# Kernel tuning notes

Measured on AMD Instinct MI355X. Metric: run time of the kernel, lower is better.

The kernel has to match this reference:

```python
import jax, jax.numpy as jnp
import numpy as np

B, P, L, H = 64, 1024, 16, 256
NUM_SIZE = 18
TOPK = min(64, P)


def _ramp(epoch, a, b):
    if epoch <= a:
        return 0.0
    if epoch >= b:
        return 1.0
    return float(epoch - a) / float(b - a)


def _normalize(x):
    return x / jnp.maximum(jnp.linalg.norm(x, axis=-1, keepdims=True), 1e-12)


def setup_inputs() -> dict:
    key = jax.random.key(0)
    ks = jax.random.split(key, 16)
    return {
        'pred_center': jax.random.normal(ks[0], (B, P, 3), dtype=jnp.float32),
        'pred_size': jax.random.uniform(ks[1], (B, P, 3), minval=0.2, maxval=1.0, dtype=jnp.float32),
        'bbox_feature': jax.random.normal(ks[2], (B, P, H), dtype=jnp.float32),
        'objectness_scores': jax.random.normal(ks[3], (B, P, 2), dtype=jnp.float32),
        'lang_emb': jax.random.normal(ks[4], (B * L, H), dtype=jnp.float32),
        'lang_num': jax.random.randint(ks[5], (B,), 1, L + 1),
        'ref_center': jax.random.normal(ks[6], (B, L, 3), dtype=jnp.float32),
        'ref_size_class': jax.random.randint(ks[7], (B, L), 0, NUM_SIZE),
        'ref_size_residual': jax.random.uniform(ks[8], (B, L, 3), minval=0.0, maxval=0.2, dtype=jnp.float32),
        'mean_size_arr': jax.random.uniform(ks[9], (NUM_SIZE, 3), minval=0.3, maxval=1.5, dtype=jnp.float32),
        'W_text': jax.random.normal(ks[10], (H, H), dtype=jnp.float32) / np.sqrt(H),
        'W_pc': jax.random.normal(ks[11], (H, H), dtype=jnp.float32) / np.sqrt(H),
        'W_pc_iou': jax.random.normal(ks[12], (H, H), dtype=jnp.float32) / np.sqrt(H),
        'log_inv_tau': jnp.array([np.log(1.0 / 0.07)], dtype=jnp.float32),
        'epoch': 40,
    }


def _forward(pred_center, pred_size, bbox_feature, objectness_scores, lang_emb,
             lang_num, ref_center, ref_size_class, ref_size_residual,
             mean_size_arr, W_text, W_pc, W_pc_iou, log_inv_tau, epoch):
    b, l = ref_center.shape[:2]
    # curriculum (python scalars, epoch is a static int)
    p = _ramp(epoch, 0, 80)
    thr = 0.05 + 0.3 * p
    gamma = 1.0 + 2.0 * p
    min_tau = 0.08 - 0.04 * p

    # top-k proposals by objectness prob
    obj_prob = jax.nn.softmax(objectness_scores, axis=2)[..., 1]  # (B,P)
    _, topk_inds = jax.lax.top_k(obj_prob, TOPK)                  # (B,K)
    feat = jnp.take_along_axis(bbox_feature, topk_inds[..., None], axis=1)  # (B,K,H)
    ctr = jnp.take_along_axis(pred_center, topk_inds[..., None], axis=1)    # (B,K,3)
    sz = jnp.take_along_axis(pred_size, topk_inds[..., None], axis=1)       # (B,K,3)

    # axis-aligned 3D IoU between gt boxes (B,L) and pred boxes (B,K) -- detached
    gt_size = mean_size_arr[ref_size_class] + ref_size_residual + 0.01  # (B,L,3)
    gmin, gmax = ref_center - gt_size / 2, ref_center + gt_size / 2
    pmin, pmax = ctr - sz / 2, ctr + sz / 2
    lo = jnp.maximum(gmin[:, :, None], pmin[:, None])   # (B,L,K,3)
    hi = jnp.minimum(gmax[:, :, None], pmax[:, None])
    inter = jnp.prod(jnp.clip(hi - lo, 0.0, None), axis=-1)  # (B,L,K)
    vol_g = jnp.prod(gt_size, axis=-1)[:, :, None]
    vol_p = jnp.prod(sz, axis=-1)[:, None]
    iou = jax.lax.stop_gradient(inter / (vol_g + vol_p - inter + 1e-7))  # (B,L,K)

    # soft target over proposals (detached)
    w = jnp.clip(iou, 0.0, None) ** gamma * (iou >= thr).astype(iou.dtype)
    onehot = jax.nn.one_hot(jnp.argmax(iou, axis=-1), TOPK, dtype=iou.dtype)
    w = jnp.where(w.sum(-1, keepdims=True) < 1e-6, onehot, w)
    target = w / (w.sum(-1, keepdims=True) + 1e-6)  # (B,L,K)

    # temperature
    inv_tau = jnp.minimum(jnp.exp(log_inv_tau)[0], 100.0)
    inv_tau = jnp.minimum(inv_tau, 1.0 / max(min_tau, 1e-6))

    # language-box contrastive
    text = _normalize(lang_emb.reshape(b, l, -1) @ W_text.T)  # (B,L,H)
    boxf = _normalize(feat @ W_pc.T)                          # (B,K,H)
    sim = jnp.einsum('blh,bkh->blk', text, boxf)              # (B,L,K)
    logp = jax.nn.log_softmax(sim * inv_tau, axis=-1)
    t2 = target / (target.sum(-1, keepdims=True) + 1e-6)      # soft_ce renorm
    ce = -(t2 * logp).sum(-1)                                 # (B,L)

    neg = iou < 0.05
    s_neg = jnp.max(jnp.where(neg, sim, -jnp.inf), axis=-1)
    s_pos = (sim * target).sum(-1)
    rank = jnp.where(neg.any(-1), jax.nn.relu(0.2 - s_pos + s_neg), 0.0)
    lang_con = ce + 0.5 * rank                                # (B,L)

    mask = (jnp.arange(l)[None, :] < lang_num[:, None]).astype(sim.dtype)
    lang_loss = (lang_con * mask).sum() / b

    # iou-aware box-box contrastive
    tm = w[..., :, None] * w[..., None, :]                    # (B,L,K,K) detached
    tm = tm / (tm.sum(-1, keepdims=True) + 1e-6)
    tm = tm / (tm.sum(-1, keepdims=True) + 1e-6)              # soft_ce renorm
    boxf_iou = _normalize(feat @ W_pc_iou.T)                  # (B,K,H)
    sim_iou = jnp.einsum('bkh,bmh->bkm', boxf_iou, boxf_iou)  # (B,K,K)
    logp_iou = jax.nn.log_softmax(sim_iou * inv_tau, axis=-1)
    iou_ce = -(tm * logp_iou[:, None]).sum(-1).mean(-1)       # (B,L)
    iou_loss = (iou_ce * mask).sum() / b

    return jnp.stack([lang_loss, iou_loss])


def reference(pred_center, pred_size, bbox_feature, objectness_scores, lang_emb,
              lang_num, ref_center, ref_size_class, ref_size_residual,
              mean_size_arr, W_text, W_pc, W_pc_iou, log_inv_tau, epoch):
    return _forward(pred_center, pred_size, bbox_feature, objectness_scores,
                    lang_emb, lang_num, ref_center, ref_size_class,
                    ref_size_residual, mean_size_arr, W_text, W_pc, W_pc_iou,
                    log_inv_tau, epoch)
```

## Files before the change

### kernel.cpp

```cpp
#include <hip/hip_runtime.h>
#include <math.h>

#define B 64
#define P 1024
#define L 16
#define H 256
#define K 64

__device__ __forceinline__ float wsum(float v){
  #pragma unroll
  for (int o = 32; o >= 1; o >>= 1) v += __shfl_xor(v, o, 64);
  return v;
}
__device__ __forceinline__ float wmaxr(float v){
  #pragma unroll
  for (int o = 32; o >= 1; o >>= 1) v = fmaxf(v, __shfl_xor(v, o, 64));
  return v;
}
__device__ __forceinline__ void wargmax(float &v, int &i){
  #pragma unroll
  for (int o = 32; o >= 1; o >>= 1){
    float v2 = __shfl_xor(v, o, 64);
    int   i2 = __shfl_xor(i, o, 64);
    if (v2 > v || (v2 == v && i2 < i)){ v = v2; i = i2; }
  }
}
__device__ __forceinline__ unsigned fkey(float f){
  unsigned b = __float_as_uint(f);
  return (b & 0x80000000u) ? ~b : (b | 0x80000000u);
}
__device__ __forceinline__ float dot4(float4 a, float4 b){
  return a.x*b.x + a.y*b.y + a.z*b.z + a.w*b.w;
}
__device__ __forceinline__ int gsw(int r){ return (r ^ (r >> 3)) & 7; }

__global__ __launch_bounds__(256) void k_topk_iou(
    const float* __restrict__ pred_center, const float* __restrict__ pred_size,
    const float* __restrict__ obj, const float* __restrict__ ref_center,
    const int* __restrict__ ref_cls, const float* __restrict__ ref_res,
    const float* __restrict__ mean_sz, const int* __restrict__ epoch_p,
    const int* __restrict__ lang_num,
    int* __restrict__ inds, float* __restrict__ iou_ws, float* __restrict__ w_ws,
    float* __restrict__ c_ws, float* __restrict__ t_ws, float* __restrict__ t2_ws,
    float* __restrict__ t2s_ws)
{
  __shared__ int hist[256];
  __shared__ int s_digit, s_cum;
  __shared__ int waveTot[4];
  __shared__ int sel[K];
  __shared__ float ctrS[K][3], szS[K][3];
  int b = blockIdx.x, tid = threadIdx.x, lane = tid & 63, wave = tid >> 6;

  const float4* o4 = (const float4*)(obj + (size_t)b*P*2);
  float4 va = o4[tid*2], vb = o4[tid*2+1];
  unsigned kj[4] = { fkey(va.y - va.x), fkey(va.w - va.z),
                     fkey(vb.y - vb.x), fkey(vb.w - vb.z) };

  unsigned prefix = 0; int rem = K;
  for (int pass = 0; pass < 4; ++pass){
    int shift = 24 - pass*8;
    hist[tid] = 0;
    __syncthreads();
    #pragma unroll
    for (int j = 0; j < 4; ++j){
      unsigned kk = kj[j];
      bool cand = (pass == 0) || ((kk >> (shift + 8)) == prefix);
      if (cand) atomicAdd(&hist[(kk >> shift) & 0xff], 1);
    }
    __syncthreads();
    int d = 255 - tid;
    int h = hist[d];
    int s = h;
    #pragma unroll
    for (int o = 1; o < 64; o <<= 1){ int t = __shfl_up(s, o, 64); if (lane >= o) s += t; }
    if (lane == 63) waveTot[wave] = s;
    __syncthreads();
    #pragma unroll
    for (int q = 0; q < 3; ++q) if (q < wave) s += waveTot[q];
    if (s >= rem && s - h < rem){ s_digit = d; s_cum = s - h; }
    __syncthreads();
    prefix = (prefix << 8) | (unsigned)s_digit;
    rem -= s_cum;
    __syncthreads();
  }
  unsigned T = prefix;
  int remFinal = rem;

  int eqc = 0;
  #pragma unroll
  for (int j = 0; j < 4; ++j) eqc += (kj[j] == T) ? 1 : 0;
  int v = eqc;
  #pragma unroll
  for (int o = 1; o < 64; o <<= 1){ int t = __shfl_up(v, o, 64); if (lane >= o) v += t; }
  if (lane == 63) waveTot[wave] = v;
  __syncthreads();
  int off = 0;
  for (int q = 0; q < wave; ++q) off += waveTot[q];
  int e = off + v - eqc;
  __syncthreads();

  int selc = 0; bool ch[4];
  #pragma unroll
  for (int j = 0; j < 4; ++j){
    bool g = kj[j] > T;
    bool q = (kj[j] == T) && (e < remFinal);
    if (kj[j] == T) e++;
    ch[j] = g || q; selc += ch[j] ? 1 : 0;
  }
  v = selc;
  #pragma unroll
  for (int o = 1; o < 64; o <<= 1){ int t = __shfl_up(v, o, 64); if (lane >= o) v += t; }
  if (lane == 63) waveTot[wave] = v;
  __syncthreads();
  off = 0;
  for (int q = 0; q < wave; ++q) off += waveTot[q];
  int slot = off + v - selc;
  #pragma unroll
  for (int j = 0; j < 4; ++j) if (ch[j]) sel[slot++] = tid*4 + j;
  __syncthreads();

  if (tid < K){
    int idx = sel[tid];
    inds[b*K + tid] = idx;
    #pragma unroll
    for (int dd = 0; dd < 3; ++dd){
      ctrS[tid][dd] = pred_center[((size_t)b*P + idx)*3 + dd];
      szS [tid][dd] = pred_size [((size_t)b*P + idx)*3 + dd];
    }
  }
  __syncthreads();

  int ep = epoch_p[0];
  float pr = ep <= 0 ? 0.f : (ep >= 80 ? 1.f : ep / 80.f);
  float thr = 0.05f + 0.3f * pr;
  float gamma = 1.f + 2.f * pr;
  int ln = lang_num[b];

  for (int l = wave; l < L; l += 4){
    int cls = ref_cls[b*L + l];
    float gs[3], gc[3]; float volg = 1.f;
    #pragma unroll
    for (int dd = 0; dd < 3; ++dd){
      gs[dd] = mean_sz[cls*3+dd] + ref_res[((size_t)b*L+l)*3+dd] + 0.01f;
      gc[dd] = ref_center[((size_t)b*L+l)*3+dd];
      volg *= gs[dd];
    }
    int k = lane;
    float inter = 1.f, volp = 1.f;
    #pragma unroll
    for (int dd = 0; dd < 3; ++dd){
      float pc = ctrS[k][dd], ps = szS[k][dd];
      float lo = fmaxf(gc[dd]-gs[dd]*0.5f, pc-ps*0.5f);
      float hi = fminf(gc[dd]+gs[dd]*0.5f, pc+ps*0.5f);
      inter *= fmaxf(hi-lo, 0.f);
      volp *= ps;
    }
    float iou = inter / (volg + volp - inter + 1e-7f);
    float wv = (iou >= thr) ? powf(iou, gamma) : 0.f;
    float S = wsum(wv);
    float av = iou; int ai = k;
    wargmax(av, ai);
    float wfin = (S < 1e-6f) ? ((k == ai) ? 1.f : 0.f) : wv;
    iou_ws[((size_t)b*L + l)*K + k] = iou;
    w_ws  [((size_t)b*L + l)*K + k] = wfin;
    float Sf = (S < 1e-6f) ? 1.f : S;
    float a = wfin * Sf;
    float c = wfin / ((a + 1e-6f) * (a/(a + 1e-6f) + 1e-6f));
    c_ws[((size_t)b*L + l)*K + k] = (l < ln) ? c : 0.f;
    float target = wfin / (Sf + 1e-6f);
    float tsum = Sf / (Sf + 1e-6f);
    float t2 = target / (tsum + 1e-6f);
    t_ws [((size_t)b*L + l)*K + k] = target;
    t2_ws[((size_t)b*L + l)*K + k] = t2;
    float T2S = wsum(t2);
    if (lane == 0) t2s_ws[b*L + l] = T2S;
  }
}

__global__ __launch_bounds__(256) void k_gemm(
    const float* __restrict__ bbox_feature, const int* __restrict__ inds,
    const float* __restrict__ lang_emb,
    const float* __restrict__ Wpc, const float* __restrict__ Wpci,
    const float* __restrict__ Wtext,
    float* __restrict__ boxr, float* __restrict__ boxri, float* __restrict__ texr)
{
  __shared__ float As[32][68], Ws[32][68];
  int gb = blockIdx.x;
  const float *W; float *C; int m0; bool gat;
  if (gb < 64)       { W = Wpc;   C = boxr;  m0 = gb*64;       gat = true;  }
  else if (gb < 128) { W = Wpci;  C = boxri; m0 = (gb-64)*64;  gat = true;  }
  else               { W = Wtext; C = texr;  m0 = (gb-128)*64; gat = false; }
  int bcol = blockIdx.y * 64;
  int tid = threadIdx.x;
  int lr = tid >> 2, lc = (tid & 3) * 4;
  int tr = tid >> 4, tc = tid & 15;
  int r = m0 + lr;
  const float* Arow = gat ? bbox_feature + ((size_t)(r >> 6)*P + inds[r])*H
                          : lang_emb + (size_t)r*H;
  const float* Wrow = W + (size_t)(bcol + lr)*H;
  float acc[4][4] = {};
  for (int h0 = 0; h0 < H; h0 += 32){
    float4 av  = *(const float4*)&Arow[h0 + lc];
    float4 av2 = *(const float4*)&Arow[h0 + 16 + lc];
    float4 wv  = *(const float4*)&Wrow[h0 + lc];
    float4 wv2 = *(const float4*)&Wrow[h0 + 16 + lc];
    As[lc+0][lr]=av.x;  As[lc+1][lr]=av.y;  As[lc+2][lr]=av.z;  As[lc+3][lr]=av.w;
    As[16+lc+0][lr]=av2.x; As[16+lc+1][lr]=av2.y; As[16+lc+2][lr]=av2.z; As[16+lc+3][lr]=av2.w;
    Ws[lc+0][lr]=wv.x;  Ws[lc+1][lr]=wv.y;  Ws[lc+2][lr]=wv.z;  Ws[lc+3][lr]=wv.w;
    Ws[16+lc+0][lr]=wv2.x; Ws[16+lc+1][lr]=wv2.y; Ws[16+lc+2][lr]=wv2.z; Ws[16+lc+3][lr]=wv2.w;
    __syncthreads();
    #pragma unroll
    for (int h = 0; h < 32; ++h){
      float4 a = *(const float4*)&As[h][tr*4];
      float4 w = *(const float4*)&Ws[h][tc*4];
      float aa[4] = {a.x,a.y,a.z,a.w};
      float ww[4] = {w.x,w.y,w.z,w.w};
      #pragma unroll
      for (int i = 0; i < 4; ++i)
        #pragma unroll
        for (int j = 0; j < 4; ++j) acc[i][j] += aa[i]*ww[j];
    }
    __syncthreads();
  }
  #pragma unroll
  for (int i = 0; i < 4; ++i){
    float4 v = make_float4(acc[i][0],acc[i][1],acc[i][2],acc[i][3]);
    *(float4*)&C[(size_t)(m0+tr*4+i)*H + bcol + tc*4] = v;
  }
}

__global__ __launch_bounds__(512) void k_contrast(
    const float* __restrict__ texr, const float* __restrict__ boxr,
    const float* __restrict__ boxri,
    const float* __restrict__ iou_ws, const float* __restrict__ w_ws,
    const float* __restrict__ c_ws, const float* __restrict__ t_ws,
    const float* __restrict__ t2_ws, const float* __restrict__ t2s_ws,
    const int* __restrict__ lang_num, const float* __restrict__ log_inv_tau,
    const int* __restrict__ epoch_p, float* __restrict__ part)
{
  extern __shared__ __align__(16) float smem[];
  int tid = threadIdx.x, lane = tid & 63, wave = tid >> 6;
  int ep = epoch_p[0];
  float pr = ep <= 0 ? 0.f : (ep >= 80 ? 1.f : ep / 80.f);
  float min_tau = fmaxf(0.08f - 0.04f*pr, 1e-6f);
  float itau = fminf(fminf(expf(log_inv_tau[0]), 100.f), 1.f/min_tau);

  if (blockIdx.x < 64){
    int b = blockIdx.x;
    float4* TB = (float4*)smem;
    float4* TT = (float4*)smem + 4096;
    const float4* srcB = (const float4*)(boxr + (size_t)b*K*H);
    const float4* srcT = (const float4*)(texr + (size_t)b*L*H);
    #pragma unroll
    for (int j = 0; j < 8; ++j){
      int i4 = tid + 512*j;
      int row = i4 >> 6, c = i4 & 63;
      TB[row*64 + (c ^ gsw(row))] = srcB[i4];
    }
    #pragma unroll
    for (int j = 0; j < 2; ++j){
      int i4 = tid + 512*j;
      int row = i4 >> 6, c = i4 & 63;
      TT[row*64 + (c ^ gsw(row))] = srcT[i4];
    }
    __syncthreads();

    int l0 = wave*2;
    float acc[2] = {0,0}, nt2[2] = {0,0};
    float nb2 = 0.f;
    for (int c = 0; c < 64; ++c){
      float4 bx = TB[lane*64 + (c ^ gsw(lane))];
      nb2 += dot4(bx, bx);
      #pragma unroll
      for (int i = 0; i < 2; ++i){
        int l = l0 + i;
        float4 tv = TT[l*64 + (c ^ gsw(l))];
        acc[i] += dot4(tv, bx);
        nt2[i] += dot4(tv, tv);
      }
    }
    float nb = fmaxf(sqrtf(nb2), 1e-12f);
    int ln = lang_num[b];
    float bacc = 0.f;
    #pragma unroll
    for (int i = 0; i < 2; ++i){
      int l = l0 + i;
      if (l < ln){
        float sv = acc[i] / (fmaxf(sqrtf(nt2[i]), 1e-12f) * nb);
        float target = t_ws [((size_t)b*L + l)*K + lane];
        float t2     = t2_ws[((size_t)b*L + l)*K + lane];
        float iou    = iou_ws[((size_t)b*L + l)*K + lane];
        float T2S    = t2s_ws[b*L + l];
        float z = sv * itau;
        float zmax = wmaxr(z);
        float se = wsum(expf(z - zmax));
        float t2z = wsum(t2 * z);
        float ce = -t2z + (zmax + logf(se)) * T2S;
        bool neg = iou < 0.05f;
        float sneg = wmaxr(neg ? sv : -INFINITY);
        int anyneg = __any(neg);
        float spos = wsum(sv * target);
        float rank = anyneg ? fmaxf(0.2f - spos + sneg, 0.f) : 0.f;
        bacc += ce + 0.5f*rank;
      }
    }
    if (lane == 0) part[blockIdx.x*8 + wave] = bacc;
  } else {
    int idx = blockIdx.x - 64;
    int b = idx >> 1, half = idx & 1;
    int r0 = half*32 + wave*4;
    float4* TI = (float4*)smem;
    float*  cL = smem + 16384;
    const float4* srcI = (const float4*)(boxri + (size_t)b*K*H);
    #pragma unroll
    for (int j = 0; j < 8; ++j){
      int i4 = tid + 512*j;
      int row = i4 >> 6, c = i4 & 63;
      TI[row*64 + (c ^ gsw(row))] = srcI[i4];
    }
    {
      int l = tid >> 5, kk = tid & 31;
      cL[l*32 + kk] = c_ws[((size_t)b*L + l)*K + half*32 + kk];
    }
    float wl[16];
    #pragma unroll
    for (int l = 0; l < 16; ++l) wl[l] = w_ws[((size_t)b*L + l)*K + lane];
    __syncthreads();

    float acc[4] = {0,0,0,0};
    float nm2 = 0.f;
    for (int c = 0; c < 64; ++c){
      float4 bx = TI[lane*64 + (c ^ gsw(lane))];
      nm2 += dot4(bx, bx);
      #pragma unroll
      for (int i = 0; i < 4; ++i){
        float4 kq = TI[(r0+i)*64 + (c ^ gsw(r0+i))];
        acc[i] += dot4(kq, bx);
      }
    }
    float4 Mv = make_float4(0.f,0.f,0.f,0.f);
    #pragma unroll
    for (int l = 0; l < 16; ++l){
      float4 cq = *(const float4*)&cL[l*32 + wave*4];
      Mv.x += cq.x * wl[l]; Mv.y += cq.y * wl[l];
      Mv.z += cq.z * wl[l]; Mv.w += cq.w * wl[l];
    }
    float Ma[4] = {Mv.x, Mv.y, Mv.z, Mv.w};
    float nm = fmaxf(sqrtf(nm2), 1e-12f);
    float contrib = 0.f;
    #pragma unroll
    for (int i = 0; i < 4; ++i){
      float nk = __shfl(nm, r0 + i, 64);
      float sv = acc[i] / (nk * nm);
      float z = sv * itau;
      float zmax = wmaxr(z);
      float se = wsum(expf(z - zmax));
      float lp = z - zmax - logf(se);
      contrib += Ma[i] * lp;
    }
    float bacc = -wsum(contrib) * (1.f/64.f);
    if (lane == 0) part[512 + idx*8 + wave] = bacc;
  }
}

__global__ __launch_bounds__(256) void k_final(const float* __restrict__ part,
                                               float* __restrict__ out)
{
  __shared__ float redI[4], redL[4];
  int tid = threadIdx.x, lane = tid & 63, wave = tid >> 6;
  float vl = part[tid] + part[256+tid];
  float vi = part[512+tid] + part[768+tid] + part[1024+tid] + part[1280+tid];
  vi = wsum(vi);
  vl = wsum(vl);
  if (lane == 0){ redI[wave] = vi; redL[wave] = vl; }
  __syncthreads();
  if (tid == 0){
    out[0] = (redL[0]+redL[1]+redL[2]+redL[3]) * (1.f/64.f);
    out[1] = (redI[0]+redI[1]+redI[2]+redI[3]) * (1.f/64.f);
  }
}

extern "C" void kernel_launch(void* const* d_in, const int* in_sizes, int n_in,
                              void* d_out, int out_size, void* d_ws, size_t ws_size,
                              hipStream_t stream)
{
  const float* pred_center = (const float*)d_in[0];
  const float* pred_size   = (const float*)d_in[1];
  const float* bbox_feature= (const float*)d_in[2];
  const float* obj         = (const float*)d_in[3];
  const float* lang_emb    = (const float*)d_in[4];
  const int*   lang_num    = (const int*)d_in[5];
  const float* ref_center  = (const float*)d_in[6];
  const int*   ref_cls     = (const int*)d_in[7];
  const float* ref_res     = (const float*)d_in[8];
  const float* mean_sz     = (const float*)d_in[9];
  const float* Wtext       = (const float*)d_in[10];
  const float* Wpc         = (const float*)d_in[11];
  const float* Wpci        = (const float*)d_in[12];
  const float* lit         = (const float*)d_in[13];
  const int*   epoch       = (const int*)d_in[14];

  float* ws = (float*)d_ws;
  int*   inds   = (int*)ws;
  float* iou_ws = ws + 4096;
  float* w_ws   = iou_ws + B*L*K;
  float* c_ws   = w_ws + B*L*K;
  float* t_ws   = c_ws + B*L*K;
  float* t2_ws  = t_ws + B*L*K;
  float* t2s_ws = t2_ws + B*L*K;
  float* texr   = t2s_ws + B*L;
  float* boxr   = texr + (size_t)B*L*H;
  float* boxri  = boxr + (size_t)B*K*H;
  float* part   = boxri + (size_t)B*K*H;

  k_topk_iou<<<B, 256, 0, stream>>>(pred_center, pred_size, obj, ref_center,
                                    ref_cls, ref_res, mean_sz, epoch, lang_num,
                                    inds, iou_ws, w_ws, c_ws, t_ws, t2_ws, t2s_ws);
  k_gemm<<<dim3(144, 4), 256, 0, stream>>>(bbox_feature, inds, lang_emb,
                                           Wpc, Wpci, Wtext, boxr, boxri, texr);
  k_contrast<<<192, 512, 81920, stream>>>(texr, boxr, boxri,
                                          iou_ws, w_ws, c_ws, t_ws, t2_ws, t2s_ws,
                                          lang_num, lit, epoch, part);
  k_final<<<1, 256, 0, stream>>>(part, (float*)d_out);
}
```

Measured before the change: 56.98 us.

## Double-buffer GEMM shared tiles and fuse final reduction via last-block counter

The GEMM kernel now uses two shared-memory buffers. The next K-slice's global loads are issued before computing on the current slice, and each iteration needs only one barrier instead of two. The separate one-block final reduction kernel is removed. Each contrast block atomically increments a counter that the top-k kernel resets, and the last block to finish reads the partial sums and writes the two outputs. This removes one launch and hides some load latency, at the cost of doubled LDS use in the GEMM and atomic/fence overhead in every contrast block.

```diff
diff --git a/kernel.cpp b/kernel.cpp
--- a/kernel.cpp
+++ b/kernel.cpp
@@ -42,7 +42,7 @@
     const int* __restrict__ lang_num,
     int* __restrict__ inds, float* __restrict__ iou_ws, float* __restrict__ w_ws,
     float* __restrict__ c_ws, float* __restrict__ t_ws, float* __restrict__ t2_ws,
-    float* __restrict__ t2s_ws)
+    float* __restrict__ t2s_ws, int* __restrict__ cnt)
 {
   __shared__ int hist[256];
   __shared__ int s_digit, s_cum;
@@ -50,6 +50,7 @@
   __shared__ int sel[K];
   __shared__ float ctrS[K][3], szS[K][3];
   int b = blockIdx.x, tid = threadIdx.x, lane = tid & 63, wave = tid >> 6;
+  if (b == 0 && tid == 0) *cnt = 0;
 
   const float4* o4 = (const float4*)(obj + (size_t)b*P*2);
   float4 va = o4[tid*2], vb = o4[tid*2+1];
@@ -184,7 +185,7 @@
     const float* __restrict__ Wtext,
     float* __restrict__ boxr, float* __restrict__ boxri, float* __restrict__ texr)
 {
-  __shared__ float As[32][68], Ws[32][68];
+  __shared__ float As[2][32][68], Ws[2][32][68];
   int gb = blockIdx.x;
   const float *W; float *C; int m0; bool gat;
   if (gb < 64)       { W = Wpc;   C = boxr;  m0 = gb*64;       gat = true;  }
@@ -199,20 +200,33 @@
                           : lang_emb + (size_t)r*H;
   const float* Wrow = W + (size_t)(bcol + lr)*H;
   float acc[4][4] = {};
+
+  {
+    float4 av  = *(const float4*)&Arow[lc];
+    float4 av2 = *(const float4*)&Arow[16 + lc];
+    float4 wv  = *(const float4*)&Wrow[lc];
+    float4 wv2 = *(const float4*)&Wrow[16 + lc];
+    As[0][lc+0][lr]=av.x;  As[0][lc+1][lr]=av.y;  As[0][lc+2][lr]=av.z;  As[0][lc+3][lr]=av.w;
+    As[0][16+lc+0][lr]=av2.x; As[0][16+lc+1][lr]=av2.y; As[0][16+lc+2][lr]=av2.z; As[0][16+lc+3][lr]=av2.w;
+    Ws[0][lc+0][lr]=wv.x;  Ws[0][lc+1][lr]=wv.y;  Ws[0][lc+2][lr]=wv.z;  Ws[0][lc+3][lr]=wv.w;
+    Ws[0][16+lc+0][lr]=wv2.x; Ws[0][16+lc+1][lr]=wv2.y; Ws[0][16+lc+2][lr]=wv2.z; Ws[0][16+lc+3][lr]=wv2.w;
+  }
+  __syncthreads();
+
+  int cur = 0;
   for (int h0 = 0; h0 < H; h0 += 32){
-    float4 av  = *(const float4*)&Arow[h0 + lc];
-    float4 av2 = *(const float4*)&Arow[h0 + 16 + lc];
-    float4 wv  = *(const float4*)&Wrow[h0 + lc];
-    float4 wv2 = *(const float4*)&Wrow[h0 + 16 + lc];
-    As[lc+0][lr]=av.x;  As[lc+1][lr]=av.y;  As[lc+2][lr]=av.z;  As[lc+3][lr]=av.w;
-    As[16+lc+0][lr]=av2.x; As[16+lc+1][lr]=av2.y; As[16+lc+2][lr]=av2.z; As[16+lc+3][lr]=av2.w;
-    Ws[lc+0][lr]=wv.x;  Ws[lc+1][lr]=wv.y;  Ws[lc+2][lr]=wv.z;  Ws[lc+3][lr]=wv.w;
-    Ws[16+lc+0][lr]=wv2.x; Ws[16+lc+1][lr]=wv2.y; Ws[16+lc+2][lr]=wv2.z; Ws[16+lc+3][lr]=wv2.w;
-    __syncthreads();
+    float4 av, av2, wv, wv2;
+    bool pre = (h0 + 32 < H);
+    if (pre){
+      av  = *(const float4*)&Arow[h0 + 32 + lc];
+      av2 = *(const float4*)&Arow[h0 + 48 + lc];
+      wv  = *(const float4*)&Wrow[h0 + 32 + lc];
+      wv2 = *(const float4*)&Wrow[h0 + 48 + lc];
+    }
     #pragma unroll
     for (int h = 0; h < 32; ++h){
-      float4 a = *(const float4*)&As[h][tr*4];
-      float4 w = *(const float4*)&Ws[h][tc*4];
+      float4 a = *(const float4*)&As[cur][h][tr*4];
+      float4 w = *(const float4*)&Ws[cur][h][tc*4];
       float aa[4] = {a.x,a.y,a.z,a.w};
       float ww[4] = {w.x,w.y,w.z,w.w};
       #pragma unroll
@@ -220,7 +234,15 @@
         #pragma unroll
         for (int j = 0; j < 4; ++j) acc[i][j] += aa[i]*ww[j];
     }
-    __syncthreads();
+    if (pre){
+      int nx = cur ^ 1;
+      As[nx][lc+0][lr]=av.x;  As[nx][lc+1][lr]=av.y;  As[nx][lc+2][lr]=av.z;  As[nx][lc+3][lr]=av.w;
+      As[nx][16+lc+0][lr]=av2.x; As[nx][16+lc+1][lr]=av2.y; As[nx][16+lc+2][lr]=av2.z; As[nx][16+lc+3][lr]=av2.w;
+      Ws[nx][lc+0][lr]=wv.x;  Ws[nx][lc+1][lr]=wv.y;  Ws[nx][lc+2][lr]=wv.z;  Ws[nx][lc+3][lr]=wv.w;
+      Ws[nx][16+lc+0][lr]=wv2.x; Ws[nx][16+lc+1][lr]=wv2.y; Ws[nx][16+lc+2][lr]=wv2.z; Ws[nx][16+lc+3][lr]=wv2.w;
+      __syncthreads();
+      cur = nx;
+    }
   }
   #pragma unroll
   for (int i = 0; i < 4; ++i){
@@ -236,9 +258,12 @@
     const float* __restrict__ c_ws, const float* __restrict__ t_ws,
     const float* __restrict__ t2_ws, const float* __restrict__ t2s_ws,
     const int* __restrict__ lang_num, const float* __restrict__ log_inv_tau,
-    const int* __restrict__ epoch_p, float* __restrict__ part)
+    const int* __restrict__ epoch_p, float* __restrict__ part,
+    int* __restrict__ cnt, float* __restrict__ out)
 {
   extern __shared__ __align__(16) float smem[];
+  __shared__ float redI[8], redL[8];
+  __shared__ int s_done;
   int tid = threadIdx.x, lane = tid & 63, wave = tid >> 6;
   int ep = epoch_p[0];
   float pr = ep <= 0 ? 0.f : (ep >= 80 ? 1.f : ep / 80.f);
@@ -304,7 +329,7 @@
         bacc += ce + 0.5f*rank;
       }
     }
-    if (lane == 0) part[blockIdx.x*8 + wave] = bacc;
+    if (lane == 0) atomicExch(&part[blockIdx.x*8 + wave], bacc);
   } else {
     int idx = blockIdx.x - 64;
     int b = idx >> 1, half = idx & 1;
@@ -359,24 +384,31 @@
       contrib += Ma[i] * lp;
     }
     float bacc = -wsum(contrib) * (1.f/64.f);
-    if (lane == 0) part[512 + idx*8 + wave] = bacc;
-  }
-}
-
-__global__ __launch_bounds__(256) void k_final(const float* __restrict__ part,
-                                               float* __restrict__ out)
-{
-  __shared__ float redI[4], redL[4];
-  int tid = threadIdx.x, lane = tid & 63, wave = tid >> 6;
-  float vl = part[tid] + part[256+tid];
-  float vi = part[512+tid] + part[768+tid] + part[1024+tid] + part[1280+tid];
-  vi = wsum(vi);
-  vl = wsum(vl);
-  if (lane == 0){ redI[wave] = vi; redL[wave] = vl; }
+    if (lane == 0) atomicExch(&part[512 + idx*8 + wave], bacc);
+  }
+
   __syncthreads();
   if (tid == 0){
-    out[0] = (redL[0]+redL[1]+redL[2]+redL[3]) * (1.f/64.f);
-    out[1] = (redI[0]+redI[1]+redI[2]+redI[3]) * (1.f/64.f);
+    __threadfence();
+    int t = atomicAdd(cnt, 1);
+    s_done = (t == 191) ? 1 : 0;
+  }
+  __syncthreads();
+  if (s_done){
+    float vl = atomicAdd(&part[tid], 0.f);
+    float vi = atomicAdd(&part[512 + tid], 0.f)
+             + atomicAdd(&part[1024 + tid], 0.f);
+    vi = wsum(vi);
+    vl = wsum(vl);
+    if (lane == 0){ redI[wave] = vi; redL[wave] = vl; }
+    __syncthreads();
+    if (tid == 0){
+      float sl = 0.f, si = 0.f;
+      #pragma unroll
+      for (int q = 0; q < 8; ++q){ sl += redL[q]; si += redI[q]; }
+      out[0] = sl * (1.f/64.f);
+      out[1] = si * (1.f/64.f);
+    }
   }
 }
 
@@ -412,14 +444,16 @@
   float* boxr   = texr + (size_t)B*L*H;
   float* boxri  = boxr + (size_t)B*K*H;
   float* part   = boxri + (size_t)B*K*H;
+  int*   cnt    = (int*)(part + 1536);
 
   k_topk_iou<<<B, 256, 0, stream>>>(pred_center, pred_size, obj, ref_center,
                                     ref_cls, ref_res, mean_sz, epoch, lang_num,
-                                    inds, iou_ws, w_ws, c_ws, t_ws, t2_ws, t2s_ws);
+                                    inds, iou_ws, w_ws, c_ws, t_ws, t2_ws, t2s_ws,
+                                    cnt);
   k_gemm<<<dim3(144, 4), 256, 0, stream>>>(bbox_feature, inds, lang_emb,
                                            Wpc, Wpci, Wtext, boxr, boxri, texr);
   k_contrast<<<192, 512, 81920, stream>>>(texr, boxr, boxri,
                                           iou_ws, w_ws, c_ws, t_ws, t2_ws, t2s_ws,
-                                          lang_num, lit, epoch, part);
-  k_final<<<1, 256, 0, stream>>>(part, (float*)d_out);
-}
+                                          lang_num, lit, epoch, part, cnt,
+                                          (float*)d_out);
+}
```

New measurement: 58.90 us. 1.03x slower.
